# Performance work log

Measured on AMD Instinct MI355X. Metric: run time of the kernel, lower is better.

## Reference

```python
import jax, jax.numpy as jnp
import numpy as np
import math

DIM = 4096
N_HEADS = 32
HEAD_DIM = DIM // N_HEADS
BSZ = 2
SEQLEN = 2048
MAX_SEQ = 2048


def _make_freqs_cis(seqlen, head_dim, theta=10000.0):
    # (seqlen, head_dim//2, 2) packed as (cos, sin) pairs, like complex rotary freqs
    inv = 1.0 / (theta ** (np.arange(0, head_dim, 2).astype(np.float32) / head_dim))
    t = np.arange(seqlen, dtype=np.float32)
    ang = np.outer(t, inv)  # (seqlen, head_dim//2)
    return jnp.asarray(np.stack([np.cos(ang), np.sin(ang)], axis=-1))


def setup_inputs() -> dict:
    key = jax.random.key(0)
    ks = jax.random.split(key, 6)
    scale = 1.0 / math.sqrt(DIM)
    x = jax.random.normal(ks[0], (BSZ, SEQLEN, DIM), dtype=jnp.float32)
    wq = jax.random.normal(ks[1], (DIM, DIM), dtype=jnp.float32) * scale
    wk = jax.random.normal(ks[2], (DIM, DIM), dtype=jnp.float32) * scale
    wv = jax.random.normal(ks[3], (DIM, DIM), dtype=jnp.float32) * scale
    wo = jax.random.normal(ks[4], (DIM, DIM), dtype=jnp.float32) * scale
    freqs_cis = _make_freqs_cis(SEQLEN, HEAD_DIM)
    # causal mask (1,1,S,S): 0 on/below diagonal, large negative above
    mask = jnp.triu(jnp.full((SEQLEN, SEQLEN), -1e9, dtype=jnp.float32), k=1)[None, None]
    hidden_state = jnp.zeros((2, BSZ, MAX_SEQ, N_HEADS, HEAD_DIM), dtype=jnp.float32)
    return {"x": x, "freqs_cis": freqs_cis, "mask": mask, "hidden_state": hidden_state,
            "wq": wq, "wk": wk, "wv": wv, "wo": wo, "start_pos": 0}


def _apply_rotary(x, freqs_cis):
    # x: (b, s, h, d); freqs_cis: (s, d//2, 2) as (cos, sin)
    b, s, h, d = x.shape
    xr = x.astype(jnp.float32).reshape(b, s, h, d // 2, 2)
    fc = freqs_cis.reshape(1, s, 1, d // 2, 2)
    real = xr[..., 0] * fc[..., 0] - xr[..., 1] * fc[..., 1]
    imag = xr[..., 0] * fc[..., 1] + xr[..., 1] * fc[..., 0]
    return jnp.stack([real, imag], axis=-1).reshape(b, s, h, d).astype(x.dtype)


def reference(x, freqs_cis, mask, hidden_state, wq, wk, wv, wo, start_pos):
    bsz, seqlen, dim = x.shape
    h, hd = N_HEADS, HEAD_DIM
    xq = (x @ wq.T).reshape(bsz, seqlen, h, hd)
    xk = (x @ wk.T).reshape(bsz, seqlen, h, hd)
    xv = (x @ wv.T).reshape(bsz, seqlen, h, hd)
    xq = _apply_rotary(xq, freqs_cis)
    xk = _apply_rotary(xk, freqs_cis)
    # KV-cache write at static start_pos
    new_k = hidden_state[0].at[:bsz, start_pos:start_pos + seqlen].set(xk)
    new_v = hidden_state[1].at[:bsz, start_pos:start_pos + seqlen].set(xv)
    new_hidden = jnp.stack([new_k, new_v], axis=0)
    keys = new_k[:bsz, :start_pos + seqlen]      # (b, kv, h, hd)
    values = new_v[:bsz, :start_pos + seqlen]
    # attention
    scores = jnp.einsum('bqhd,bkhd->bhqk', xq, keys) / math.sqrt(hd)
    scores = scores + mask
    probs = jax.nn.softmax(scores.astype(jnp.float32), axis=-1).astype(xq.dtype)
    out = jnp.einsum('bhqk,bkhd->bqhd', probs, values).reshape(bsz, seqlen, h * hd)
    return out @ wo.T, new_hidden
```

## Files before the change

kernel.cpp:

```cpp
#include <hip/hip_runtime.h>
#include <hip/hip_bf16.h>

#define DIM   4096
#define SEQ   2048
#define NH    32
#define HD    128
#define BSZ   2
#define SEG   16777216

typedef unsigned short u16;
typedef unsigned int   u32;
typedef __attribute__((ext_vector_type(8))) short bf16x8;
typedef __attribute__((ext_vector_type(4))) float f32x4;
typedef __attribute__((ext_vector_type(4))) u16   u16x4;

__device__ __forceinline__ float b2f(u16 u) {
    union { u32 i; float f; } c; c.i = ((u32)u) << 16; return c.f;
}
__device__ __forceinline__ u16 f2b(float f) {
    u32 x = __float_as_uint(f);
    return (u16)((x + 0x7FFFu + ((x >> 16) & 1u)) >> 16);
}
__device__ __forceinline__ void gload_lds16(const void* g, void* l) {
    __builtin_amdgcn_global_load_lds(
        (__attribute__((address_space(1))) void*)(unsigned long)(g),
        (__attribute__((address_space(3))) void*)(l), 16, 0, 0);
}

__global__ __launch_bounds__(256) void cast5(const float* __restrict__ x,
                                             const float* __restrict__ wq,
                                             const float* __restrict__ wk,
                                             const float* __restrict__ wv,
                                             const float* __restrict__ wo,
                                             u16* __restrict__ dst) {
    int i = blockIdx.x * 1024 + threadIdx.x * 4;
    int seg = i >> 24;
    int off = i & (SEG - 1);
    const float* s = x;
    if (seg == 1) s = wq; else if (seg == 2) s = wk;
    else if (seg == 3) s = wv; else if (seg == 4) s = wo;
    float4 v = *(const float4*)(s + off);
    u16x4 o; o.x = f2b(v.x); o.y = f2b(v.y); o.z = f2b(v.z); o.w = f2b(v.w);
    *(u16x4*)(dst + i) = o;
}

#define BARRIER() do { asm volatile("" ::: "memory"); \
                       __builtin_amdgcn_s_barrier(); \
                       asm volatile("" ::: "memory"); } while (0)

template<int OUT_BF16>
__global__ __launch_bounds__(512, 2) void gemm8p(const u16* __restrict__ A,
                                                 const u16* __restrict__ Bbase,
                                                 void* __restrict__ Cv) {
    __shared__ __align__(16) char lds[131072];

    const int tid = threadIdx.x;
    const int lane = tid & 63, w = tid >> 6;
    const int quad = lane >> 4, m16 = lane & 15;
    const int wm = w >> 2, wn = w & 3;
    const int m0 = blockIdx.y * 256, n0 = blockIdx.x * 256;
    const u16* Bp = Bbase + (size_t)blockIdx.z * SEG;

    const u16* aSrc[2];
    const u16* bSrc[2];
#pragma unroll
    for (int i = 0; i < 2; ++i) {
        int p = i * 8192 + w * 1024 + lane * 16;
        int q = p ^ (((p >> 7) & 3) << 4);
        int rowoff = (q >> 11) * 16 + ((q >> 6) & 15);
        int coloff = (((q >> 10) & 1) << 5) + ((q & 63) >> 1);
        aSrc[i] = A  + (size_t)(m0 + rowoff) * DIM + coloff;
        bSrc[i] = Bp + (size_t)(n0 + rowoff) * DIM + coloff;
    }
    const int laneoff = m16 * 64 + ((quad * 16) ^ (((m16 >> 1) & 3) << 4));

    f32x4 acc[8][4];
#pragma unroll
    for (int a = 0; a < 8; ++a)
#pragma unroll
        for (int b = 0; b < 4; ++b) acc[a][b] = 0.f;

    bf16x8 af[4][2];
    bf16x8 bfr[4][2];

#define STAGE_A(d, h, kt) do { int kk_ = ((kt) & 63) * 64;                       \
    gload_lds16(aSrc[0] + (size_t)(h) * (128 * DIM) + kk_,                       \
                lds + ((d) * 4 + (h)) * 16384 + w * 1024);                       \
    gload_lds16(aSrc[1] + (size_t)(h) * (128 * DIM) + kk_,                       \
                lds + ((d) * 4 + (h)) * 16384 + 8192 + w * 1024); } while (0)
#define STAGE_B(d, h, kt) do { int kk_ = ((kt) & 63) * 64;                       \
    gload_lds16(bSrc[0] + (size_t)(h) * (128 * DIM) + kk_,                       \
                lds + ((d) * 4 + 2 + (h)) * 16384 + w * 1024);                   \
    gload_lds16(bSrc[1] + (size_t)(h) * (128 * DIM) + kk_,                       \
                lds + ((d) * 4 + 2 + (h)) * 16384 + 8192 + w * 1024); } while (0)
#define LOAD_A(d, mh) do {                                                       \
    const char* base_ = lds + ((d) * 4 + wm) * 16384 + (mh) * 8192 + laneoff;    \
    _Pragma("unroll") for (int mt = 0; mt < 4; ++mt)                             \
    _Pragma("unroll") for (int ks = 0; ks < 2; ++ks)                             \
        af[mt][ks] = *(const bf16x8*)(base_ + mt * 2048 + ks * 1024); } while (0)
#define LOAD_B(d, nh) do {                                                       \
    const char* base_ = lds + ((d) * 4 + 2 + (wn >> 1)) * 16384                  \
                        + (wn & 1) * 8192 + (nh) * 4096 + laneoff;               \
    _Pragma("unroll") for (int nt = 0; nt < 2; ++nt)                             \
    _Pragma("unroll") for (int ks = 0; ks < 2; ++ks)                             \
        bfr[(nh) * 2 + nt][ks] = *(const bf16x8*)(base_ + nt * 2048 + ks * 1024);\
    } while (0)
#define MFMA_Q(mh, nh) do {                                                      \
    _Pragma("unroll") for (int mt = 0; mt < 4; ++mt)                             \
    _Pragma("unroll") for (int nt = 0; nt < 2; ++nt)                             \
    _Pragma("unroll") for (int ks = 0; ks < 2; ++ks)                             \
        acc[(mh) * 4 + mt][(nh) * 2 + nt] =                                      \
            __builtin_amdgcn_mfma_f32_16x16x32_bf16(                             \
                af[mt][ks], bfr[(nh) * 2 + nt][ks],                              \
                acc[(mh) * 4 + mt][(nh) * 2 + nt], 0, 0, 0); } while (0)

    STAGE_B(0, 0, 0); STAGE_B(0, 1, 0); STAGE_A(0, 0, 0); STAGE_A(0, 1, 0);
    STAGE_B(1, 0, 1); STAGE_B(1, 1, 1);
    asm volatile("s_waitcnt vmcnt(4)" ::: "memory");
    BARRIER();

    for (int it = 0; it < 32; ++it) {
        const int t = 2 * it;
        LOAD_A(0, 0); LOAD_B(0, 0);
        STAGE_A(1, 0, t + 1);
        asm volatile("s_waitcnt lgkmcnt(8)" ::: "memory");
        BARRIER();
        asm volatile("s_waitcnt lgkmcnt(0)" ::: "memory");
        __builtin_amdgcn_s_setprio(1); MFMA_Q(0, 0); __builtin_amdgcn_s_setprio(0);
        BARRIER();
        LOAD_B(0, 1);
        STAGE_A(1, 1, t + 1);
        BARRIER();
        asm volatile("s_waitcnt lgkmcnt(0)" ::: "memory");
        __builtin_amdgcn_s_setprio(1); MFMA_Q(0, 1); __builtin_amdgcn_s_setprio(0);
        BARRIER();
        LOAD_A(0, 1);
        STAGE_B(0, 0, t + 2);
        BARRIER();
        asm volatile("s_waitcnt lgkmcnt(0)" ::: "memory");
        __builtin_amdgcn_s_setprio(1); MFMA_Q(1, 1); __builtin_amdgcn_s_setprio(0);
        BARRIER();
        STAGE_B(0, 1, t + 2);
        BARRIER();
        __builtin_amdgcn_s_setprio(1); MFMA_Q(1, 0); __builtin_amdgcn_s_setprio(0);
        asm volatile("s_waitcnt vmcnt(4)" ::: "memory");
        BARRIER();
        LOAD_A(1, 0); LOAD_B(1, 0);
        STAGE_A(0, 0, t + 2);
        asm volatile("s_waitcnt lgkmcnt(8)" ::: "memory");
        BARRIER();
        asm volatile("s_waitcnt lgkmcnt(0)" ::: "memory");
        __builtin_amdgcn_s_setprio(1); MFMA_Q(0, 0); __builtin_amdgcn_s_setprio(0);
        BARRIER();
        LOAD_B(1, 1);
        STAGE_A(0, 1, t + 2);
        BARRIER();
        asm volatile("s_waitcnt lgkmcnt(0)" ::: "memory");
        __builtin_amdgcn_s_setprio(1); MFMA_Q(0, 1); __builtin_amdgcn_s_setprio(0);
        BARRIER();
        LOAD_A(1, 1);
        STAGE_B(1, 0, t + 3);
        BARRIER();
        asm volatile("s_waitcnt lgkmcnt(0)" ::: "memory");
        __builtin_amdgcn_s_setprio(1); MFMA_Q(1, 1); __builtin_amdgcn_s_setprio(0);
        BARRIER();
        STAGE_B(1, 1, t + 3);
        BARRIER();
        __builtin_amdgcn_s_setprio(1); MFMA_Q(1, 0); __builtin_amdgcn_s_setprio(0);
        asm volatile("s_waitcnt vmcnt(4)" ::: "memory");
        BARRIER();
    }
    asm volatile("s_waitcnt vmcnt(0)" ::: "memory");

#pragma unroll
    for (int mt = 0; mt < 8; ++mt)
#pragma unroll
        for (int nt = 0; nt < 4; ++nt) {
            const int row = m0 + wm * 128 + mt * 16 + quad * 4;
            const int col = n0 + wn * 64 + nt * 16 + m16;
            if (OUT_BF16) {
                u16* C = (u16*)Cv + (size_t)blockIdx.z * SEG;
#pragma unroll
                for (int r = 0; r < 4; ++r)
                    C[(size_t)(row + r) * DIM + col] = f2b(acc[mt][nt][r]);
            } else {
                float* C = (float*)Cv + (size_t)blockIdx.z * SEG;
#pragma unroll
                for (int r = 0; r < 4; ++r)
                    C[(size_t)(row + r) * DIM + col] = acc[mt][nt][r];
            }
        }
#undef STAGE_A
#undef STAGE_B
#undef LOAD_A
#undef LOAD_B
#undef MFMA_Q
}

__global__ __launch_bounds__(256) void rope(const u16* __restrict__ XQ,
                                            const u16* __restrict__ XK,
                                            const float* __restrict__ FC,
                                            u16* __restrict__ Qo,
                                            u16* __restrict__ Ko,
                                            float* __restrict__ KH) {
    int tid = blockIdx.x * 256 + threadIdx.x;
    int i = tid & 63;
    int s = (tid >> 11) & 2047;
    float2 cs = *(const float2*)(FC + (s * 64 + i) * 2);
    u32 q = ((const u32*)XQ)[tid];
    u32 k = ((const u32*)XK)[tid];
    float q0 = b2f((u16)(q & 0xffff)), q1 = b2f((u16)(q >> 16));
    float k0 = b2f((u16)(k & 0xffff)), k1 = b2f((u16)(k >> 16));
    float qr = q0 * cs.x - q1 * cs.y, qi = q0 * cs.y + q1 * cs.x;
    float kr = k0 * cs.x - k1 * cs.y, ki = k0 * cs.y + k1 * cs.x;
    ((u32*)Qo)[tid] = (u32)f2b(qr) | ((u32)f2b(qi) << 16);
    ((u32*)Ko)[tid] = (u32)f2b(kr) | ((u32)f2b(ki) << 16);
    *(float2*)(KH + (size_t)tid * 2) = make_float2(kr, ki);
}

__global__ __launch_bounds__(256) void vprep(const u16* __restrict__ XV,
                                             float* __restrict__ VH,
                                             u16* __restrict__ VT) {
    __shared__ u16 tile[64][65];
    int bs = blockIdx.x;
    int bd = blockIdx.y;
    int bh = blockIdx.z;
    int b = bh >> 5, h = bh & 31;
    int t = threadIdx.x;
    int c = t & 63, r4 = t >> 6;
    for (int i = 0; i < 16; ++i) {
        int sr = i * 4 + r4;
        int gi = ((b * SEQ + bs * 64 + sr) * NH + h) * HD + bd * 64 + c;
        u16 v = XV[gi];
        VH[gi] = b2f(v);
        tile[sr][c] = v;
    }
    __syncthreads();
    for (int i = 0; i < 16; ++i) {
        int dr = i * 4 + r4;
        VT[(bh * HD + bd * 64 + dr) * SEQ + bs * 64 + c] = tile[c][dr];
    }
}

__global__ __launch_bounds__(256, 2) void flash(const u16* __restrict__ Q,
                                                const u16* __restrict__ K,
                                                const u16* __restrict__ Vt,
                                                u16* __restrict__ O) {
    __shared__ __align__(16) u16 k_lds[64 * 128];
    __shared__ __align__(16) u16 v_lds[128 * 64];
    __shared__ __align__(16) u16 p_lds[4][32 * 68];

    const int tid = threadIdx.x, lane = tid & 63, w = tid >> 6;
    const int quad = lane >> 4, m16 = lane & 15;
    const int bh = blockIdx.x;
    const int b = bh >> 5, h = bh & 31;
    const int qt = (gridDim.y - 1) - blockIdx.y;
    const int q0 = qt * 128;
    const int wrow = q0 + w * 32;

    const int gk = w * 256 + lane;
    bf16x8 qa[2][4];
#pragma unroll
    for (int mt = 0; mt < 2; ++mt) {
        const u16* qp = Q + ((size_t)(b * SEQ + wrow + mt * 16 + m16) * NH + h) * HD;
#pragma unroll
        for (int ks = 0; ks < 4; ++ks) qa[mt][ks] = *(const bf16x8*)(qp + ks * 32 + quad * 8);
    }

    float mi[2][4], li[2][4];
    f32x4 o[2][8];
#pragma unroll
    for (int mt = 0; mt < 2; ++mt)
#pragma unroll
        for (int r = 0; r < 4; ++r) { mi[mt][r] = -1e30f; li[mt][r] = 0.f; }
#pragma unroll
    for (int mt = 0; mt < 2; ++mt)
#pragma unroll
        for (int n = 0; n < 8; ++n) o[mt][n] = 0.f;

    const float scale = 0.08838834764831845f;
    const int nkt = 2 * qt + 2;

    const u16* Kbase = K + ((size_t)(b * SEQ) * NH + h) * HD;
    const u16* Vbase = Vt + (size_t)(bh * HD) * SEQ;

    for (int kt = 0; kt < nkt; ++kt) {
        const int k0 = kt * 64;
        __syncthreads();
#pragma unroll
        for (int j = 0; j < 4; ++j) {
            int g = gk + j * 64;
            int r = g >> 4, p = g & 15, c = p ^ (r & 15);
            gload_lds16(Kbase + (size_t)(k0 + r) * DIM + c * 8,
                        (char*)k_lds + w * 4096 + j * 1024);
        }
#pragma unroll
        for (int j = 0; j < 4; ++j) {
            int g = gk + j * 64;
            int r = g >> 3, p = g & 7, c = p ^ (r & 7);
            gload_lds16(Vbase + (size_t)r * SEQ + k0 + c * 8,
                        (char*)v_lds + w * 4096 + j * 1024);
        }
        __syncthreads();

        if (k0 > wrow + 31) continue;

        f32x4 s[2][4];
#pragma unroll
        for (int mt = 0; mt < 2; ++mt)
#pragma unroll
            for (int nt = 0; nt < 4; ++nt) s[mt][nt] = 0.f;
#pragma unroll
        for (int ks = 0; ks < 4; ++ks)
#pragma unroll
            for (int nt = 0; nt < 4; ++nt) {
                int rk = nt * 16 + m16;
                int p = (ks * 4 + quad) ^ m16;
                bf16x8 kb = *(const bf16x8*)(k_lds + rk * 128 + p * 8);
#pragma unroll
                for (int mt = 0; mt < 2; ++mt)
                    s[mt][nt] = __builtin_amdgcn_mfma_f32_16x16x32_bf16(
                        qa[mt][ks], kb, s[mt][nt], 0, 0, 0);
            }

#pragma unroll
        for (int mt = 0; mt < 2; ++mt) {
            float sv[4][4];
            const bool need_mask = (k0 + 63) > (wrow + mt * 16);
#pragma unroll
            for (int nt = 0; nt < 4; ++nt)
#pragma unroll
                for (int r = 0; r < 4; ++r) {
                    float v = s[mt][nt][r] * scale;
                    if (need_mask) {
                        int col = k0 + nt * 16 + m16;
                        int rq = wrow + mt * 16 + quad * 4 + r;
                        if (col > rq) v = -1e30f;
                    }
                    sv[nt][r] = v;
                }
#pragma unroll
            for (int r = 0; r < 4; ++r) {
                float mx = fmaxf(fmaxf(sv[0][r], sv[1][r]), fmaxf(sv[2][r], sv[3][r]));
#pragma unroll
                for (int off = 8; off >= 1; off >>= 1) mx = fmaxf(mx, __shfl_xor(mx, off));
                float mnew = fmaxf(mi[mt][r], mx);
                float alpha = __expf(mi[mt][r] - mnew);
                float sum = 0.f;
#pragma unroll
                for (int nt = 0; nt < 4; ++nt) {
                    float pv = __expf(sv[nt][r] - mnew);
                    sum += pv;
                    p_lds[w][(mt * 16 + quad * 4 + r) * 68 + nt * 16 + m16] = f2b(pv);
                }
#pragma unroll
                for (int off = 8; off >= 1; off >>= 1) sum += __shfl_xor(sum, off);
                li[mt][r] = li[mt][r] * alpha + sum;
                mi[mt][r] = mnew;
#pragma unroll
                for (int n8 = 0; n8 < 8; ++n8) o[mt][n8][r] *= alpha;
            }
        }

        asm volatile("s_waitcnt lgkmcnt(0)" ::: "memory");

#pragma unroll
        for (int ks2 = 0; ks2 < 2; ++ks2) {
            bf16x8 pa[2];
#pragma unroll
            for (int mt = 0; mt < 2; ++mt)
                pa[mt] = *(const bf16x8*)(&p_lds[w][0] + (mt * 16 + m16) * 68 + ks2 * 32 + quad * 8);
#pragma unroll
            for (int n8 = 0; n8 < 8; ++n8) {
                int rv = n8 * 16 + m16;
                int p = (ks2 * 4 + quad) ^ (m16 & 7);
                bf16x8 vb = *(const bf16x8*)(v_lds + rv * 64 + p * 8);
#pragma unroll
                for (int mt = 0; mt < 2; ++mt)
                    o[mt][n8] = __builtin_amdgcn_mfma_f32_16x16x32_bf16(
                        pa[mt], vb, o[mt][n8], 0, 0, 0);
            }
        }
    }

#pragma unroll
    for (int mt = 0; mt < 2; ++mt) {
        float inv[4];
#pragma unroll
        for (int r = 0; r < 4; ++r) inv[r] = 1.0f / li[mt][r];
#pragma unroll
        for (int n8 = 0; n8 < 8; ++n8)
#pragma unroll
            for (int r = 0; r < 4; ++r) {
                int rq = wrow + mt * 16 + quad * 4 + r;
                O[((size_t)(b * SEQ + rq) * NH + h) * HD + n8 * 16 + m16] =
                    f2b(o[mt][n8][r] * inv[r]);
            }
    }
}

extern "C" void kernel_launch(void* const* d_in, const int* in_sizes, int n_in,
                              void* d_out, int out_size, void* d_ws, size_t ws_size,
                              hipStream_t stream) {
    const float* x  = (const float*)d_in[0];
    const float* fc = (const float*)d_in[1];
    const float* wq = (const float*)d_in[4];
    const float* wk = (const float*)d_in[5];
    const float* wv = (const float*)d_in[6];
    const float* wo = (const float*)d_in[7];

    float* out = (float*)d_out;
    float* kh  = out + 16777216;
    float* vh  = out + 33554432;

    u16* ws = (u16*)d_ws;
    u16* xb  = ws + 0L * SEG;
    u16* wqb = ws + 1L * SEG;
    u16* wkb = ws + 2L * SEG;
    u16* wvb = ws + 3L * SEG;
    u16* wob = ws + 4L * SEG;
    u16* xqb = ws + 5L * SEG;
    u16* xkb = ws + 6L * SEG;
    u16* xvb = ws + 7L * SEG;
    u16* qro = xb;
    u16* kro = wqb;
    u16* vt  = wkb;
    u16* ao  = wvb;

    cast5<<<dim3(81920), dim3(256), 0, stream>>>(x, wq, wk, wv, wo, ws);
    gemm8p<1><<<dim3(16, 16, 3), dim3(512), 0, stream>>>(xb, wqb, (void*)xqb);
    rope<<<dim3(32768), dim3(256), 0, stream>>>(xqb, xkb, fc, qro, kro, kh);
    vprep<<<dim3(32, 2, 64), dim3(256), 0, stream>>>(xvb, vh, vt);
    flash<<<dim3(64, 16), dim3(256), 0, stream>>>(qro, kro, vt, ao);
    gemm8p<0><<<dim3(16, 16, 1), dim3(512), 0, stream>>>(ao, wob, (void*)out);
}
```

Before: 1.119 ms.

## Use 32x32x16 MFMA in GEMM and register-prefetch K/V tiles in attention

The GEMM kernel moves from 16x16x32 to 32x32x16 bf16 MFMA tiles, with new fragment addressing and a new epilogue, so each LDS fragment feeds more math and fewer instructions are issued. The attention kernel stops using direct global-to-LDS loads. It now prefetches the next K/V tile into registers while the current tile is computed, then writes those registers to LDS. The GEMM change risks LDS bank conflicts under the existing swizzle. The attention prefetch adds register pressure and an extra register-to-LDS store step.

```diff
diff --git a/kernel.cpp b/kernel.cpp
--- a/kernel.cpp
+++ b/kernel.cpp
@@ -12,6 +12,7 @@
 typedef unsigned int   u32;
 typedef __attribute__((ext_vector_type(8))) short bf16x8;
 typedef __attribute__((ext_vector_type(4))) float f32x4;
+typedef __attribute__((ext_vector_type(16))) float f32x16;
 typedef __attribute__((ext_vector_type(4))) u16   u16x4;
 
 __device__ __forceinline__ float b2f(u16 u) {
@@ -26,6 +27,10 @@
         (__attribute__((address_space(1))) void*)(unsigned long)(g),
         (__attribute__((address_space(3))) void*)(l), 16, 0, 0);
 }
+
+#define BARRIER() do { asm volatile("" ::: "memory"); \
+                       __builtin_amdgcn_s_barrier(); \
+                       asm volatile("" ::: "memory"); } while (0)
 
 __global__ __launch_bounds__(256) void cast5(const float* __restrict__ x,
                                              const float* __restrict__ wq,
@@ -44,10 +49,6 @@
     *(u16x4*)(dst + i) = o;
 }
 
-#define BARRIER() do { asm volatile("" ::: "memory"); \
-                       __builtin_amdgcn_s_barrier(); \
-                       asm volatile("" ::: "memory"); } while (0)
-
 template<int OUT_BF16>
 __global__ __launch_bounds__(512, 2) void gemm8p(const u16* __restrict__ A,
                                                  const u16* __restrict__ Bbase,
@@ -56,7 +57,10 @@
 
     const int tid = threadIdx.x;
     const int lane = tid & 63, w = tid >> 6;
-    const int quad = lane >> 4, m16 = lane & 15;
+    const int l31 = lane & 31;
+    const int r16 = lane & 15;
+    const int g32 = (lane >> 4) & 1;
+    const int kh8 = lane >> 5;
     const int wm = w >> 2, wn = w & 3;
     const int m0 = blockIdx.y * 256, n0 = blockIdx.x * 256;
     const u16* Bp = Bbase + (size_t)blockIdx.z * SEG;
@@ -72,16 +76,19 @@
         aSrc[i] = A  + (size_t)(m0 + rowoff) * DIM + coloff;
         bSrc[i] = Bp + (size_t)(n0 + rowoff) * DIM + coloff;
     }
-    const int laneoff = m16 * 64 + ((quad * 16) ^ (((m16 >> 1) & 3) << 4));
-
-    f32x4 acc[8][4];
-#pragma unroll
-    for (int a = 0; a < 8; ++a)
-#pragma unroll
-        for (int b = 0; b < 4; ++b) acc[a][b] = 0.f;
-
-    bf16x8 af[4][2];
-    bf16x8 bfr[4][2];
+    const int rgoff = g32 * 2048 + r16 * 64;
+    const int xsw   = (r16 >> 1) & 3;
+    const int gA    = ((kh8)     ^ xsw) * 16;
+    const int gB    = ((2 | kh8) ^ xsw) * 16;
+
+    f32x16 acc[4][2];
+#pragma unroll
+    for (int a = 0; a < 4; ++a)
+#pragma unroll
+        for (int b = 0; b < 2; ++b) acc[a][b] = 0.f;
+
+    bf16x8 af[2][4];
+    bf16x8 bfr[2][4];
 
 #define STAGE_A(d, h, kt) do { int kk_ = ((kt) & 63) * 64;                       \
     gload_lds16(aSrc[0] + (size_t)(h) * (128 * DIM) + kk_,                       \
@@ -94,25 +101,24 @@
     gload_lds16(bSrc[1] + (size_t)(h) * (128 * DIM) + kk_,                       \
                 lds + ((d) * 4 + 2 + (h)) * 16384 + 8192 + w * 1024); } while (0)
 #define LOAD_A(d, mh) do {                                                       \
-    const char* base_ = lds + ((d) * 4 + wm) * 16384 + (mh) * 8192 + laneoff;    \
-    _Pragma("unroll") for (int mt = 0; mt < 4; ++mt)                             \
-    _Pragma("unroll") for (int ks = 0; ks < 2; ++ks)                             \
-        af[mt][ks] = *(const bf16x8*)(base_ + mt * 2048 + ks * 1024); } while (0)
+    const char* base_ = lds + ((d) * 4 + wm) * 16384 + (mh) * 8192 + rgoff;      \
+    _Pragma("unroll") for (int m2 = 0; m2 < 2; ++m2) {                           \
+        af[m2][0] = *(const bf16x8*)(base_ + m2 * 4096 + gA);                    \
+        af[m2][1] = *(const bf16x8*)(base_ + m2 * 4096 + gB);                    \
+        af[m2][2] = *(const bf16x8*)(base_ + m2 * 4096 + 1024 + gA);             \
+        af[m2][3] = *(const bf16x8*)(base_ + m2 * 4096 + 1024 + gB); } } while (0)
 #define LOAD_B(d, nh) do {                                                       \
     const char* base_ = lds + ((d) * 4 + 2 + (wn >> 1)) * 16384                  \
-                        + (wn & 1) * 8192 + (nh) * 4096 + laneoff;               \
-    _Pragma("unroll") for (int nt = 0; nt < 2; ++nt)                             \
-    _Pragma("unroll") for (int ks = 0; ks < 2; ++ks)                             \
-        bfr[(nh) * 2 + nt][ks] = *(const bf16x8*)(base_ + nt * 2048 + ks * 1024);\
-    } while (0)
+                        + (wn & 1) * 8192 + (nh) * 4096 + rgoff;                 \
+        bfr[nh][0] = *(const bf16x8*)(base_ + gA);                               \
+        bfr[nh][1] = *(const bf16x8*)(base_ + gB);                               \
+        bfr[nh][2] = *(const bf16x8*)(base_ + 1024 + gA);                        \
+        bfr[nh][3] = *(const bf16x8*)(base_ + 1024 + gB); } while (0)
 #define MFMA_Q(mh, nh) do {                                                      \
-    _Pragma("unroll") for (int mt = 0; mt < 4; ++mt)                             \
-    _Pragma("unroll") for (int nt = 0; nt < 2; ++nt)                             \
-    _Pragma("unroll") for (int ks = 0; ks < 2; ++ks)                             \
-        acc[(mh) * 4 + mt][(nh) * 2 + nt] =                                      \
-            __builtin_amdgcn_mfma_f32_16x16x32_bf16(                             \
-                af[mt][ks], bfr[(nh) * 2 + nt][ks],                              \
-                acc[(mh) * 4 + mt][(nh) * 2 + nt], 0, 0, 0); } while (0)
+    _Pragma("unroll") for (int m2 = 0; m2 < 2; ++m2)                             \
+    _Pragma("unroll") for (int ks = 0; ks < 4; ++ks)                             \
+        acc[(mh) * 2 + m2][nh] = __builtin_amdgcn_mfma_f32_32x32x16_bf16(        \
+            af[m2][ks], bfr[nh][ks], acc[(mh) * 2 + m2][nh], 0, 0, 0); } while (0)
 
     STAGE_B(0, 0, 0); STAGE_B(0, 1, 0); STAGE_A(0, 0, 0); STAGE_A(0, 1, 0);
     STAGE_B(1, 0, 1); STAGE_B(1, 1, 1);
@@ -173,21 +179,24 @@
     asm volatile("s_waitcnt vmcnt(0)" ::: "memory");
 
 #pragma unroll
-    for (int mt = 0; mt < 8; ++mt)
-#pragma unroll
-        for (int nt = 0; nt < 4; ++nt) {
-            const int row = m0 + wm * 128 + mt * 16 + quad * 4;
-            const int col = n0 + wn * 64 + nt * 16 + m16;
-            if (OUT_BF16) {
-                u16* C = (u16*)Cv + (size_t)blockIdx.z * SEG;
-#pragma unroll
-                for (int r = 0; r < 4; ++r)
-                    C[(size_t)(row + r) * DIM + col] = f2b(acc[mt][nt][r]);
-            } else {
-                float* C = (float*)Cv + (size_t)blockIdx.z * SEG;
-#pragma unroll
-                for (int r = 0; r < 4; ++r)
-                    C[(size_t)(row + r) * DIM + col] = acc[mt][nt][r];
+    for (int mt = 0; mt < 4; ++mt)
+#pragma unroll
+        for (int nt = 0; nt < 2; ++nt) {
+            const int col = n0 + wn * 64 + nt * 32 + l31;
+#pragma unroll
+            for (int q4 = 0; q4 < 4; ++q4) {
+                const int row = m0 + wm * 128 + mt * 32 + q4 * 8 + kh8 * 4;
+                if (OUT_BF16) {
+                    u16* C = (u16*)Cv + (size_t)blockIdx.z * SEG;
+#pragma unroll
+                    for (int r = 0; r < 4; ++r)
+                        C[(size_t)(row + r) * DIM + col] = f2b(acc[mt][nt][q4 * 4 + r]);
+                } else {
+                    float* C = (float*)Cv + (size_t)blockIdx.z * SEG;
+#pragma unroll
+                    for (int r = 0; r < 4; ++r)
+                        C[(size_t)(row + r) * DIM + col] = acc[mt][nt][q4 * 4 + r];
+                }
             }
         }
 #undef STAGE_A
@@ -258,7 +267,20 @@
     const int q0 = qt * 128;
     const int wrow = q0 + w * 32;
 
-    const int gk = w * 256 + lane;
+    const u16* Kbase = K + ((size_t)(b * SEQ) * NH + h) * HD;
+    const u16* Vbase = Vt + (size_t)(bh * HD) * SEQ;
+
+    const u16* ksrc[4];
+    const u16* vsrc[4];
+#pragma unroll
+    for (int j = 0; j < 4; ++j) {
+        int g = w * 256 + lane + j * 64;
+        int rK = g >> 4, cK = (g & 15) ^ (rK & 15);
+        ksrc[j] = Kbase + (size_t)rK * DIM + cK * 8;
+        int rV = g >> 3, cV = (g & 7) ^ (rV & 7);
+        vsrc[j] = Vbase + (size_t)rV * SEQ + cV * 8;
+    }
+
     bf16x8 qa[2][4];
 #pragma unroll
     for (int mt = 0; mt < 2; ++mt) {
@@ -281,104 +303,110 @@
     const float scale = 0.08838834764831845f;
     const int nkt = 2 * qt + 2;
 
-    const u16* Kbase = K + ((size_t)(b * SEQ) * NH + h) * HD;
-    const u16* Vbase = Vt + (size_t)(bh * HD) * SEQ;
+    uint4 kreg[4], vreg[4];
+#pragma unroll
+    for (int j = 0; j < 4; ++j) {
+        kreg[j] = *(const uint4*)(ksrc[j]);
+        vreg[j] = *(const uint4*)(vsrc[j]);
+    }
 
     for (int kt = 0; kt < nkt; ++kt) {
         const int k0 = kt * 64;
-        __syncthreads();
+        asm volatile("s_waitcnt vmcnt(0)" ::: "memory");
+        asm volatile("s_waitcnt lgkmcnt(0)" ::: "memory");
+        BARRIER();
 #pragma unroll
         for (int j = 0; j < 4; ++j) {
-            int g = gk + j * 64;
-            int r = g >> 4, p = g & 15, c = p ^ (r & 15);
-            gload_lds16(Kbase + (size_t)(k0 + r) * DIM + c * 8,
-                        (char*)k_lds + w * 4096 + j * 1024);
+            *(uint4*)((char*)k_lds + w * 4096 + j * 1024 + lane * 16) = kreg[j];
+            *(uint4*)((char*)v_lds + w * 4096 + j * 1024 + lane * 16) = vreg[j];
         }
-#pragma unroll
-        for (int j = 0; j < 4; ++j) {
-            int g = gk + j * 64;
-            int r = g >> 3, p = g & 7, c = p ^ (r & 7);
-            gload_lds16(Vbase + (size_t)r * SEQ + k0 + c * 8,
-                        (char*)v_lds + w * 4096 + j * 1024);
-        }
-        __syncthreads();
-
-        if (k0 > wrow + 31) continue;
-
-        f32x4 s[2][4];
-#pragma unroll
-        for (int mt = 0; mt < 2; ++mt)
-#pragma unroll
-            for (int nt = 0; nt < 4; ++nt) s[mt][nt] = 0.f;
-#pragma unroll
-        for (int ks = 0; ks < 4; ++ks)
-#pragma unroll
-            for (int nt = 0; nt < 4; ++nt) {
-                int rk = nt * 16 + m16;
-                int p = (ks * 4 + quad) ^ m16;
-                bf16x8 kb = *(const bf16x8*)(k_lds + rk * 128 + p * 8);
-#pragma unroll
-                for (int mt = 0; mt < 2; ++mt)
-                    s[mt][nt] = __builtin_amdgcn_mfma_f32_16x16x32_bf16(
-                        qa[mt][ks], kb, s[mt][nt], 0, 0, 0);
-            }
-
-#pragma unroll
-        for (int mt = 0; mt < 2; ++mt) {
-            float sv[4][4];
-            const bool need_mask = (k0 + 63) > (wrow + mt * 16);
-#pragma unroll
-            for (int nt = 0; nt < 4; ++nt)
-#pragma unroll
-                for (int r = 0; r < 4; ++r) {
-                    float v = s[mt][nt][r] * scale;
-                    if (need_mask) {
-                        int col = k0 + nt * 16 + m16;
-                        int rq = wrow + mt * 16 + quad * 4 + r;
-                        if (col > rq) v = -1e30f;
-                    }
-                    sv[nt][r] = v;
-                }
-#pragma unroll
-            for (int r = 0; r < 4; ++r) {
-                float mx = fmaxf(fmaxf(sv[0][r], sv[1][r]), fmaxf(sv[2][r], sv[3][r]));
-#pragma unroll
-                for (int off = 8; off >= 1; off >>= 1) mx = fmaxf(mx, __shfl_xor(mx, off));
-                float mnew = fmaxf(mi[mt][r], mx);
-                float alpha = __expf(mi[mt][r] - mnew);
-                float sum = 0.f;
-#pragma unroll
-                for (int nt = 0; nt < 4; ++nt) {
-                    float pv = __expf(sv[nt][r] - mnew);
-                    sum += pv;
-                    p_lds[w][(mt * 16 + quad * 4 + r) * 68 + nt * 16 + m16] = f2b(pv);
-                }
-#pragma unroll
-                for (int off = 8; off >= 1; off >>= 1) sum += __shfl_xor(sum, off);
-                li[mt][r] = li[mt][r] * alpha + sum;
-                mi[mt][r] = mnew;
-#pragma unroll
-                for (int n8 = 0; n8 < 8; ++n8) o[mt][n8][r] *= alpha;
+        if (kt + 1 < nkt) {
+            const int kn = (kt + 1) * 64;
+#pragma unroll
+            for (int j = 0; j < 4; ++j) {
+                kreg[j] = *(const uint4*)(ksrc[j] + (size_t)kn * DIM);
+                vreg[j] = *(const uint4*)(vsrc[j] + kn);
             }
         }
-
-        asm volatile("s_waitcnt lgkmcnt(0)" ::: "memory");
-
-#pragma unroll
-        for (int ks2 = 0; ks2 < 2; ++ks2) {
-            bf16x8 pa[2];
+        asm volatile("s_waitcnt lgkmcnt(0)" ::: "memory");
+        BARRIER();
+
+        if (k0 <= wrow + 31) {
+            f32x4 s[2][4];
 #pragma unroll
             for (int mt = 0; mt < 2; ++mt)
-                pa[mt] = *(const bf16x8*)(&p_lds[w][0] + (mt * 16 + m16) * 68 + ks2 * 32 + quad * 8);
-#pragma unroll
-            for (int n8 = 0; n8 < 8; ++n8) {
-                int rv = n8 * 16 + m16;
-                int p = (ks2 * 4 + quad) ^ (m16 & 7);
-                bf16x8 vb = *(const bf16x8*)(v_lds + rv * 64 + p * 8);
+#pragma unroll
+                for (int nt = 0; nt < 4; ++nt) s[mt][nt] = 0.f;
+#pragma unroll
+            for (int ks = 0; ks < 4; ++ks)
+#pragma unroll
+                for (int nt = 0; nt < 4; ++nt) {
+                    int rk = nt * 16 + m16;
+                    int p = (ks * 4 + quad) ^ m16;
+                    bf16x8 kb = *(const bf16x8*)(k_lds + rk * 128 + p * 8);
+#pragma unroll
+                    for (int mt = 0; mt < 2; ++mt)
+                        s[mt][nt] = __builtin_amdgcn_mfma_f32_16x16x32_bf16(
+                            qa[mt][ks], kb, s[mt][nt], 0, 0, 0);
+                }
+
+#pragma unroll
+            for (int mt = 0; mt < 2; ++mt) {
+                float sv[4][4];
+                const bool need_mask = (k0 + 63) > (wrow + mt * 16);
+#pragma unroll
+                for (int nt = 0; nt < 4; ++nt)
+#pragma unroll
+                    for (int r = 0; r < 4; ++r) {
+                        float v = s[mt][nt][r] * scale;
+                        if (need_mask) {
+                            int col = k0 + nt * 16 + m16;
+                            int rq = wrow + mt * 16 + quad * 4 + r;
+                            if (col > rq) v = -1e30f;
+                        }
+                        sv[nt][r] = v;
+                    }
+#pragma unroll
+                for (int r = 0; r < 4; ++r) {
+                    float mx = fmaxf(fmaxf(sv[0][r], sv[1][r]), fmaxf(sv[2][r], sv[3][r]));
+#pragma unroll
+                    for (int off = 8; off >= 1; off >>= 1) mx = fmaxf(mx, __shfl_xor(mx, off));
+                    float mnew = fmaxf(mi[mt][r], mx);
+                    float alpha = __expf(mi[mt][r] - mnew);
+                    float sum = 0.f;
+#pragma unroll
+                    for (int nt = 0; nt < 4; ++nt) {
+                        float pv = __expf(sv[nt][r] - mnew);
+                        sum += pv;
+                        p_lds[w][(mt * 16 + quad * 4 + r) * 68 + nt * 16 + m16] = f2b(pv);
+                    }
+#pragma unroll
+                    for (int off = 8; off >= 1; off >>= 1) sum += __shfl_xor(sum, off);
+                    li[mt][r] = li[mt][r] * alpha + sum;
+                    mi[mt][r] = mnew;
+#pragma unroll
+                    for (int n8 = 0; n8 < 8; ++n8) o[mt][n8][r] *= alpha;
+                }
+            }
+
+            asm volatile("s_waitcnt lgkmcnt(0)" ::: "memory");
+
+#pragma unroll
+            for (int ks2 = 0; ks2 < 2; ++ks2) {
+                bf16x8 pa[2];
 #pragma unroll
                 for (int mt = 0; mt < 2; ++mt)
-                    o[mt][n8] = __builtin_amdgcn_mfma_f32_16x16x32_bf16(
-                        pa[mt], vb, o[mt][n8], 0, 0, 0);
+                    pa[mt] = *(const bf16x8*)(&p_lds[w][0] + (mt * 16 + m16) * 68 + ks2 * 32 + quad * 8);
+#pragma unroll
+                for (int n8 = 0; n8 < 8; ++n8) {
+                    int rv = n8 * 16 + m16;
+                    int p = (ks2 * 4 + quad) ^ (m16 & 7);
+                    bf16x8 vb = *(const bf16x8*)(v_lds + rv * 64 + p * 8);
+#pragma unroll
+                    for (int mt = 0; mt < 2; ++mt)
+                        o[mt][n8] = __builtin_amdgcn_mfma_f32_16x16x32_bf16(
+                            pa[mt], vb, o[mt][n8], 0, 0, 0);
+                }
             }
         }
     }
```

Result: slower. 1.252 ms (+11.9%).
